# Performance work log

Hardware: AMD Instinct MI355X
Metric: run time of the kernel (lower is better)

## Reference

```python
import jax, jax.numpy as jnp
import numpy as np
import math

N_HEAD = 12


def setup_inputs() -> dict:
    key = jax.random.key(0)
    k1, k2, k3 = jax.random.split(key, 3)
    B, T, C = 4, 2048, 768
    x = jax.random.normal(k1, (B, T, C), dtype=jnp.float32)
    W = jax.random.normal(k2, (C, 3 * C), dtype=jnp.float32) * 0.02
    b = jax.random.normal(k3, (3 * C,), dtype=jnp.float32) * 0.02
    return {"x": x, "W": W, "b": b}


def reference(x, W, b):
    B, T, C = x.shape
    H = N_HEAD
    d = C // H
    qkv = x @ W + b                                # [B,T,3C]
    q, k, v = jnp.split(qkv, 3, axis=-1)           # each [B,T,C]
    q = q.reshape(B, T, H, d).transpose(0, 2, 1, 3)  # [B,H,T,d]
    k = k.reshape(B, T, H, d).transpose(0, 2, 1, 3)
    v = v.reshape(B, T, H, d).transpose(0, 2, 1, 3)
    # NOTE: source multiplies by sqrt(d) (not divides) -- faithful reproduction.
    att = jnp.einsum('bhqd,bhkd->bhqk', q, k) * (1.0 * math.sqrt(d))
    causal = jnp.tril(jnp.ones((T, T), dtype=bool))  # [T,T]
    att = jnp.where(causal[None, None, :, :], att, -jnp.inf)
    att = jax.nn.softmax(att, axis=-1)
    y = jnp.einsum('bhqk,bhkd->bhqd', att, v)      # [B,H,T,d]
    y = y.transpose(0, 2, 1, 3).reshape(B, T, C)   # [B,T,C]
    return y
```

## Files before the change

kernel.cpp:

```cpp
#include <hip/hip_runtime.h>
#include <math.h>

#define B_ 4
#define T_ 2048
#define C_ 768
#define H_ 12
#define D_ 64
#define N3C (3*C_)
#define BH_ (B_*H_)
#define QSCALE 11.5415603f

typedef float f32x4 __attribute__((ext_vector_type(4)));
typedef _Float16 f16x8 __attribute__((ext_vector_type(8)));
typedef unsigned short ushort_t;

__device__ __forceinline__ void async16(const void* g, void* l) {
    __builtin_amdgcn_global_load_lds(
        (const __attribute__((address_space(1))) unsigned int*)(g),
        (__attribute__((address_space(3))) unsigned int*)(l),
        16, 0, 0);
}

__device__ __forceinline__ unsigned pk_f16(float a, float b) {
    __fp16 r2[2];
    *(__fp16 __attribute__((ext_vector_type(2)))*)r2 = __builtin_amdgcn_cvt_pkrtz(a, b);
    return *(unsigned*)r2;
}

__global__ __launch_bounds__(256) void conv_xw(const float* __restrict__ x,
                                               const float* __restrict__ W,
                                               _Float16* __restrict__ Xh,
                                               _Float16* __restrict__ Wh)
{
    __shared__ float tile[64][65];
    int bid = blockIdx.x;
    int tid = threadIdx.x;
    if (bid < 3072) {
        int idx = bid * 256 + tid;
        const float4 a = *reinterpret_cast<const float4*>(&x[(size_t)idx * 8]);
        const float4 b = *reinterpret_cast<const float4*>(&x[(size_t)idx * 8 + 4]);
        f16x8 o = {(_Float16)a.x, (_Float16)a.y, (_Float16)a.z, (_Float16)a.w,
                   (_Float16)b.x, (_Float16)b.y, (_Float16)b.z, (_Float16)b.w};
        *reinterpret_cast<f16x8*>(&Xh[(size_t)idx * 8]) = o;
    } else {
        int b2 = bid - 3072;
        int n0 = (b2 % 36) * 64, k0 = (b2 / 36) * 64;
        #pragma unroll
        for (int t = 0; t < 16; ++t) {
            int c = t * 256 + tid;
            int kr = c >> 6, nc = c & 63;
            tile[kr][nc] = W[(size_t)(k0 + kr) * N3C + n0 + nc];
        }
        __syncthreads();
        #pragma unroll
        for (int t = 0; t < 16; ++t) {
            int c = t * 256 + tid;
            int nr = c >> 6, kc = c & 63;
            Wh[(size_t)(n0 + nr) * C_ + k0 + kc] = (_Float16)tile[kc][nr];
        }
    }
}

__global__ __launch_bounds__(256) void qkv_gemm(const _Float16* __restrict__ Xh,
                                                const _Float16* __restrict__ Wh,
                                                const float* __restrict__ bias,
                                                _Float16* __restrict__ Qf,
                                                _Float16* __restrict__ Kf,
                                                _Float16* __restrict__ Vt)
{
    __shared__ __align__(16) ushort_t SMEM[2 * 2 * 128 * 64];

    int tid = threadIdx.x, lane = tid & 63, w = tid >> 6;
    int wm = w >> 1, wn = w & 1;
    int l15 = lane & 15, l4 = lane >> 4;
    int srow = lane >> 3;
    int scol = (((lane & 7) ^ srow)) << 3;

    int wg = blockIdx.x;
    int l = (wg & 7) * 144 + (wg >> 3);
    int mt = l / 18, nt = l % 18;
    int row0 = mt * 128, col0 = nt * 128;

    f32x4 acc[4][4];
    #pragma unroll
    for (int i = 0; i < 4; ++i)
        #pragma unroll
        for (int j = 0; j < 4; ++j)
            acc[i][j] = f32x4{0.f, 0.f, 0.f, 0.f};

    #pragma unroll
    for (int j = 0; j < 4; ++j) {
        int rowb = w * 32 + j * 8;
        async16(Xh + (size_t)(row0 + rowb + srow) * C_ + scol, &SMEM[rowb * 64]);
        async16(Wh + (size_t)(col0 + rowb + srow) * C_ + scol, &SMEM[8192 + rowb * 64]);
    }
    __syncthreads();

    int cur = 0;
    for (int it = 0; it < 12; ++it) {
        int nxt = cur ^ 1;
        int k0n = (it + 1) * 64;
        bool pf = (it + 1 < 12);
        const char* AsC = (const char*)(SMEM + cur * 16384);
        const char* BsC = AsC + 16384;
        ushort_t* An = SMEM + nxt * 16384;
        ushort_t* Bn = An + 8192;

        if (pf) {
            #pragma unroll
            for (int j = 0; j < 2; ++j) {
                int rowb = w * 32 + j * 8;
                async16(Xh + (size_t)(row0 + rowb + srow) * C_ + k0n + scol, &An[rowb * 64]);
                async16(Wh + (size_t)(col0 + rowb + srow) * C_ + k0n + scol, &Bn[rowb * 64]);
            }
        }
        f16x8 bfr[4][2];
        #pragma unroll
        for (int n = 0; n < 4; ++n) {
            int r = wn * 64 + n * 16 + l15;
            #pragma unroll
            for (int kk = 0; kk < 2; ++kk)
                bfr[n][kk] = *reinterpret_cast<const f16x8*>(BsC + r * 128 + ((kk * 64 + l4 * 16) ^ ((r & 7) << 4)));
        }
        {
            f16x8 af[2][2];
            #pragma unroll
            for (int m = 0; m < 2; ++m) {
                int r = wm * 64 + m * 16 + l15;
                #pragma unroll
                for (int kk = 0; kk < 2; ++kk)
                    af[m][kk] = *reinterpret_cast<const f16x8*>(AsC + r * 128 + ((kk * 64 + l4 * 16) ^ ((r & 7) << 4)));
            }
            #pragma unroll
            for (int kk = 0; kk < 2; ++kk)
                #pragma unroll
                for (int m = 0; m < 2; ++m)
                    #pragma unroll
                    for (int n = 0; n < 4; ++n)
                        acc[m][n] = __builtin_amdgcn_mfma_f32_16x16x32_f16(af[m][kk], bfr[n][kk], acc[m][n], 0, 0, 0);
        }

        if (pf) {
            #pragma unroll
            for (int j = 2; j < 4; ++j) {
                int rowb = w * 32 + j * 8;
                async16(Xh + (size_t)(row0 + rowb + srow) * C_ + k0n + scol, &An[rowb * 64]);
                async16(Wh + (size_t)(col0 + rowb + srow) * C_ + k0n + scol, &Bn[rowb * 64]);
            }
        }
        {
            f16x8 af[2][2];
            #pragma unroll
            for (int m = 0; m < 2; ++m) {
                int r = wm * 64 + (m + 2) * 16 + l15;
                #pragma unroll
                for (int kk = 0; kk < 2; ++kk)
                    af[m][kk] = *reinterpret_cast<const f16x8*>(AsC + r * 128 + ((kk * 64 + l4 * 16) ^ ((r & 7) << 4)));
            }
            #pragma unroll
            for (int kk = 0; kk < 2; ++kk)
                #pragma unroll
                for (int m = 0; m < 2; ++m)
                    #pragma unroll
                    for (int n = 0; n < 4; ++n)
                        acc[m + 2][n] = __builtin_amdgcn_mfma_f32_16x16x32_f16(af[m][kk], bfr[n][kk], acc[m + 2][n], 0, 0, 0);
        }

        __syncthreads();
        cur = nxt;
    }

    char* EB = (char*)SMEM;
    int p = col0 / C_;

    if (p < 2) {
        #pragma unroll
        for (int n = 0; n < 4; ++n) {
            int col = wn * 64 + n * 16 + l15;
            float bv = bias[col0 + col];
            #pragma unroll
            for (int m = 0; m < 4; ++m) {
                #pragma unroll
                for (int r = 0; r < 4; ++r) {
                    int row = wm * 64 + m * 16 + l4 * 4 + r;
                    float v = acc[m][n][r] + bv;
                    if (p == 0) v *= QSCALE;
                    int off = row * 256 + ((col * 2) ^ ((row & 7) << 4));
                    *reinterpret_cast<_Float16*>(EB + off) = (_Float16)v;
                }
            }
        }
        __syncthreads();
        int ti = tid >> 1, half = tid & 1;
        int grow = row0 + ti;
        int bq = grow >> 11, t = grow & (T_ - 1);
        int rem = (col0 + half * 64) - p * C_;
        int hh = rem >> 6;
        _Float16* dst = (p == 0 ? Qf : Kf) + ((size_t)(bq * H_ + hh) * T_ + t) * D_;
        #pragma unroll
        for (int u = 0; u < 8; ++u) {
            int off = ti * 256 + ((half * 128 + u * 16) ^ ((ti & 7) << 4));
            *reinterpret_cast<uint4*>((char*)dst + u * 16) = *reinterpret_cast<const uint4*>(EB + off);
        }
    } else {
        #pragma unroll
        for (int n = 0; n < 4; ++n) {
            int col = wn * 64 + n * 16 + l15;
            float bv = bias[col0 + col];
            #pragma unroll
            for (int m = 0; m < 4; ++m) {
                int row = wm * 64 + m * 16 + l4 * 4;
                uint2 pk;
                pk.x = pk_f16(acc[m][n][0] + bv, acc[m][n][1] + bv);
                pk.y = pk_f16(acc[m][n][2] + bv, acc[m][n][3] + bv);
                int off = col * 256 + ((row * 2) ^ ((col & 15) << 4));
                *reinterpret_cast<uint2*>(EB + off) = pk;
            }
        }
        __syncthreads();
        int dcol = tid >> 1, half = tid & 1;
        int rem = (col0 + dcol) - 1536;
        int hh = rem >> 6, dd = rem & 63;
        int bq = row0 >> 11, t0 = row0 & (T_ - 1);
        _Float16* dst = Vt + ((size_t)(bq * H_ + hh) * D_ + dd) * T_ + t0 + half * 64;
        #pragma unroll
        for (int u = 0; u < 8; ++u) {
            int off = dcol * 256 + ((half * 128 + u * 16) ^ ((dcol & 15) << 4));
            *reinterpret_cast<uint4*>((char*)dst + u * 16) = *reinterpret_cast<const uint4*>(EB + off);
        }
    }
}

__device__ const unsigned char ITEM_QT[24] = {15,15,7,14,14,13,13,6,12,12,11,11,5,10,10,9,9,4,8,8,3,2,1,0};
__device__ const unsigned char ITEM_CH[24] = { 0, 1,0, 0, 1, 0, 1,0, 0, 1, 0, 1,0, 0, 1,0,1,0,0,1,0,0,0,0};

__global__ __launch_bounds__(256, 4) void attn(const _Float16* __restrict__ Qf,
                                               const _Float16* __restrict__ Kf,
                                               const _Float16* __restrict__ Vt,
                                               float* __restrict__ out,
                                               float* __restrict__ Op,
                                               float* __restrict__ ML)
{
    __shared__ __align__(16) char smem[40960];
    ushort_t* lds = (ushort_t*)smem;

    int tid = threadIdx.x, lane = tid & 63, w = tid >> 6;
    int l15 = lane & 15, l4 = lane >> 4;
    int bid = blockIdx.x;
    int rank = bid / BH_;
    int bh = bid % BH_;
    int qt = ITEM_QT[rank];
    int ch = ITEM_CH[rank];
    int b = bh / H_, h = bh % H_;
    int q0 = qt * 128;

    int it0 = (qt < 8 || ch == 0) ? 0 : (qt + 1);
    int it1 = (qt >= 8 && ch == 0) ? (qt + 1) : (2 * qt + 2);

    f16x8 qf[2][2];
    #pragma unroll
    for (int qs = 0; qs < 2; ++qs) {
        int q = q0 + w * 32 + qs * 16 + l15;
        const _Float16* ph = Qf + ((size_t)bh * T_ + q) * D_;
        qf[qs][0] = *reinterpret_cast<const f16x8*>(ph + l4 * 8);
        qf[qs][1] = *reinterpret_cast<const f16x8*>(ph + 32 + l4 * 8);
    }

    f32x4 yacc[2][4];
    #pragma unroll
    for (int qs = 0; qs < 2; ++qs)
        #pragma unroll
        for (int dt = 0; dt < 4; ++dt)
            yacc[qs][dt] = f32x4{0.f, 0.f, 0.f, 0.f};
    float m_run[2] = {-INFINITY, -INFINITY};
    float l_run[2] = {0.f, 0.f};

    int srow = lane >> 3;
    int scol = ((lane & 7) ^ srow) << 3;
    char* PwB = (char*)(lds + 16384 + w * 1024);
    int pswz = (l15 & 7) << 4;

    const _Float16* kp[2];
    const _Float16* vp[2];
    #pragma unroll
    for (int j = 0; j < 2; ++j) {
        int row = (w * 2 + j) * 8 + srow;
        kp[j] = Kf + ((size_t)bh * T_ + it0 * 64 + row) * D_ + scol;
        vp[j] = Vt + ((size_t)bh * D_ + row) * T_ + it0 * 64 + scol;
    }

    #pragma unroll
    for (int j = 0; j < 2; ++j) {
        ushort_t* dK = lds + (w * 2 + j) * 512;
        async16(kp[j], dK);
        async16(vp[j], dK + 4096);
        kp[j] += 64 * D_;
        vp[j] += 64;
    }
    __syncthreads();

    int cur = 0;
    for (int it = it0; it < it1; ++it) {
        int k0 = it * 64;
        int nxt = cur ^ 1;
        if (it + 1 < it1) {
            #pragma unroll
            for (int j = 0; j < 2; ++j) {
                ushort_t* dK = lds + nxt * 8192 + (w * 2 + j) * 512;
                async16(kp[j], dK);
                async16(vp[j], dK + 4096);
                kp[j] += 64 * D_;
                vp[j] += 64;
            }
        }

        if (k0 <= q0 + w * 32 + 31) {
            const char* KHc = (const char*)(lds + cur * 8192);
            const char* VSc = KHc + 8192;
            f16x8 pa[2][2];
            f32x4 sa[2][4];
            #pragma unroll
            for (int qs = 0; qs < 2; ++qs)
                #pragma unroll
                for (int i = 0; i < 4; ++i) sa[qs][i] = f32x4{0.f, 0.f, 0.f, 0.f};

            __builtin_amdgcn_s_setprio(1);
            #pragma unroll
            for (int kt = 0; kt < 4; ++kt) {
                int krow = kt * 16 + l15;
                int swz = (krow & 7) << 4;
                #pragma unroll
                for (int dh = 0; dh < 2; ++dh) {
                    f16x8 kf = *reinterpret_cast<const f16x8*>(KHc + krow * 128 + ((dh * 64 + l4 * 16) ^ swz));
                    sa[0][kt] = __builtin_amdgcn_mfma_f32_16x16x32_f16(kf, qf[0][dh], sa[0][kt], 0, 0, 0);
                    sa[1][kt] = __builtin_amdgcn_mfma_f32_16x16x32_f16(kf, qf[1][dh], sa[1][kt], 0, 0, 0);
                }
            }
            __builtin_amdgcn_s_setprio(0);

            #pragma unroll
            for (int qs = 0; qs < 2; ++qs) {
                if (it >= 2 * qt) {
                    int qg = q0 + w * 32 + qs * 16 + l15;
                    #pragma unroll
                    for (int kt = 0; kt < 4; ++kt)
                        #pragma unroll
                        for (int r = 0; r < 4; ++r)
                            if (k0 + kt * 16 + l4 * 4 + r > qg) sa[qs][kt][r] = -INFINITY;
                }

                float mx = sa[qs][0][0];
                #pragma unroll
                for (int kt = 0; kt < 4; ++kt)
                    #pragma unroll
                    for (int r = 0; r < 4; ++r) mx = fmaxf(mx, sa[qs][kt][r]);
                mx = fmaxf(mx, __shfl_xor(mx, 16));
                mx = fmaxf(mx, __shfl_xor(mx, 32));

                float mn;
                if (__all(mx <= m_run[qs] + 8.0f)) {
                    mn = m_run[qs];
                } else {
                    mn = fmaxf(m_run[qs], mx);
                    float sc = exp2f(m_run[qs] - mn);
                    m_run[qs] = mn;
                    l_run[qs] *= sc;
                    #pragma unroll
                    for (int dt = 0; dt < 4; ++dt) yacc[qs][dt] *= sc;
                }

                float p[4][4];
                float rs = 0.f;
                #pragma unroll
                for (int kt = 0; kt < 4; ++kt)
                    #pragma unroll
                    for (int r = 0; r < 4; ++r) {
                        p[kt][r] = exp2f(sa[qs][kt][r] - mn);
                        rs += p[kt][r];
                    }
                l_run[qs] += rs;

                #pragma unroll
                for (int kt = 0; kt < 4; ++kt) {
                    uint2 pw;
                    pw.x = pk_f16(p[kt][0], p[kt][1]);
                    pw.y = pk_f16(p[kt][2], p[kt][3]);
                    int off = (l15 * 128 + kt * 32 + l4 * 8) ^ pswz;
                    *reinterpret_cast<uint2*>(PwB + off) = pw;
                }
                pa[qs][0] = *reinterpret_cast<const f16x8*>(PwB + ((l15 * 128 + l4 * 16) ^ pswz));
                pa[qs][1] = *reinterpret_cast<const f16x8*>(PwB + ((l15 * 128 + 64 + l4 * 16) ^ pswz));
            }

            __builtin_amdgcn_s_setprio(1);
            #pragma unroll
            for (int dt = 0; dt < 4; ++dt) {
                int vrow = dt * 16 + l15;
                int vswz = (vrow & 7) << 4;
                #pragma unroll
                for (int kk = 0; kk < 2; ++kk) {
                    f16x8 vf = *reinterpret_cast<const f16x8*>(VSc + vrow * 128 + ((kk * 64 + l4 * 16) ^ vswz));
                    yacc[0][dt] = __builtin_amdgcn_mfma_f32_16x16x32_f16(vf, pa[0][kk], yacc[0][dt], 0, 0, 0);
                    yacc[1][dt] = __builtin_amdgcn_mfma_f32_16x16x32_f16(vf, pa[1][kk], yacc[1][dt], 0, 0, 0);
                }
            }
            __builtin_amdgcn_s_setprio(0);
        }
        __syncthreads();
        cur = nxt;
    }

    #pragma unroll
    for (int qs = 0; qs < 2; ++qs) {
        l_run[qs] += __shfl_xor(l_run[qs], 16);
        l_run[qs] += __shfl_xor(l_run[qs], 32);
    }

    float* ot = (float*)smem;
    if (qt < 8) {
        #pragma unroll
        for (int qs = 0; qs < 2; ++qs) {
            float inv = 1.0f / l_run[qs];
            int rq = w * 32 + qs * 16 + l15;
            #pragma unroll
            for (int dt = 0; dt < 4; ++dt)
                #pragma unroll
                for (int r = 0; r < 4; ++r)
                    ot[rq * 68 + dt * 16 + l4 * 4 + r] = yacc[qs][dt][r] * inv;
        }
        __syncthreads();
        int rr = tid >> 1, c0 = (tid & 1) * 32;
        size_t ob = ((size_t)(b * T_ + q0 + rr)) * C_ + h * D_ + c0;
        #pragma unroll
        for (int u = 0; u < 8; ++u) {
            float4 v = *reinterpret_cast<const float4*>(&ot[rr * 68 + c0 + u * 4]);
            *reinterpret_cast<float4*>(&out[ob + u * 4]) = v;
        }
    } else {
        #pragma unroll
        for (int qs = 0; qs < 2; ++qs) {
            int rq = w * 32 + qs * 16 + l15;
            #pragma unroll
            for (int dt = 0; dt < 4; ++dt)
                #pragma unroll
                for (int r = 0; r < 4; ++r)
                    ot[rq * 68 + dt * 16 + l4 * 4 + r] = yacc[qs][dt][r];
        }
        if (l4 == 0) {
            float* mlp = ML + (((size_t)bh * 8 + (qt - 8)) * 2 + ch) * 256;
            #pragma unroll
            for (int qs = 0; qs < 2; ++qs) {
                int ql = w * 32 + qs * 16 + l15;
                mlp[ql] = m_run[qs];
                mlp[128 + ql] = l_run[qs];
            }
        }
        __syncthreads();
        int rr = tid >> 1, c0 = (tid & 1) * 32;
        float* dst = Op + (((size_t)bh * 8 + (qt - 8)) * 2 + ch) * 8192 + rr * 64 + c0;
        #pragma unroll
        for (int u = 0; u < 8; ++u) {
            float4 v = *reinterpret_cast<const float4*>(&ot[rr * 68 + c0 + u * 4]);
            *reinterpret_cast<float4*>(&dst[u * 4]) = v;
        }
    }
}

__global__ __launch_bounds__(256) void merge(const float* __restrict__ Op,
                                             const float* __restrict__ ML,
                                             float* __restrict__ out)
{
    int gid = blockIdx.x * 256 + threadIdx.x;
    int row = gid >> 4, seg = gid & 15;
    int q = row & 127, qt8 = (row >> 7) & 7, bh = row >> 10;

    size_t mbase = ((size_t)bh * 8 + qt8) * 2 * 256;
    float m1 = ML[mbase + q],       l1 = ML[mbase + 128 + q];
    float m2 = ML[mbase + 256 + q], l2 = ML[mbase + 256 + 128 + q];
    float m = fmaxf(m1, m2);
    float a1 = exp2f(m1 - m), a2 = exp2f(m2 - m);
    float inv = 1.0f / (l1 * a1 + l2 * a2);

    size_t obase = ((size_t)bh * 8 + qt8) * 2 * 8192 + q * 64 + seg * 4;
    float4 o1 = *reinterpret_cast<const float4*>(&Op[obase]);
    float4 o2 = *reinterpret_cast<const float4*>(&Op[obase + 8192]);
    float4 r;
    r.x = (o1.x * a1 + o2.x * a2) * inv;
    r.y = (o1.y * a1 + o2.y * a2) * inv;
    r.z = (o1.z * a1 + o2.z * a2) * inv;
    r.w = (o1.w * a1 + o2.w * a2) * inv;

    int b = bh / H_, h = bh % H_;
    int t = (qt8 + 8) * 128 + q;
    *reinterpret_cast<float4*>(&out[((size_t)(b * T_ + t)) * C_ + h * D_ + seg * 4]) = r;
}

extern "C" void kernel_launch(void* const* d_in, const int* in_sizes, int n_in,
                              void* d_out, int out_size, void* d_ws, size_t ws_size,
                              hipStream_t stream)
{
    const float* x    = (const float*)d_in[0];
    const float* W    = (const float*)d_in[1];
    const float* bias = (const float*)d_in[2];

    const size_t per = (size_t)BH_ * T_ * D_;
    _Float16* Qf = (_Float16*)d_ws;
    _Float16* Kf = Qf + per;
    _Float16* Vt = Kf + per;
    _Float16* Xh = Vt + per;
    _Float16* Wh = Xh + (size_t)8192 * C_;
    float*    Op = (float*)(Wh + (size_t)N3C * C_);
    float*    ML = Op + (size_t)48 * 8 * 2 * 8192;

    conv_xw<<<dim3(3072 + 432), 256, 0, stream>>>(x, W, Xh, Wh);
    qkv_gemm<<<dim3(64 * 18), 256, 0, stream>>>(Xh, Wh, bias, Qf, Kf, Vt);
    attn<<<dim3(24 * BH_), 256, 0, stream>>>(Qf, Kf, Vt, (float*)d_out, Op, ML);
    merge<<<dim3(49152 * 16 / 256), 256, 0, stream>>>(Op, ML, (float*)d_out);
}
```

Baseline: 130.5 us.

## Permute K rows so P stays in registers, drop LDS round-trip for P

K rows are loaded into LDS in a permuted order, so each lane's QK^T accumulator values line up with the A-operand layout the PV MFMA expects. P can then be packed to f16 directly in registers instead of being written to and reread from a per-wave LDS scratch buffer. The causal mask is updated to use the permuted key indices, and LDS usage falls from 40KB to 32KB. The epilogue is also unified to use float4 swizzled LDS stores for both the split and non-split paths. The permutation must be exactly right for both the mask and the MFMA layout, otherwise results will be wrong.

New measurement: 129.5 us. No clear change (-0.8%).

```diff
diff --git a/kernel.cpp b/kernel.cpp
--- a/kernel.cpp
+++ b/kernel.cpp
@@ -241,7 +241,7 @@
                                                float* __restrict__ Op,
                                                float* __restrict__ ML)
 {
-    __shared__ __align__(16) char smem[40960];
+    __shared__ __align__(16) char smem[32768];
     ushort_t* lds = (ushort_t*)smem;
 
     int tid = threadIdx.x, lane = tid & 63, w = tid >> 6;
@@ -277,16 +277,15 @@
 
     int srow = lane >> 3;
     int scol = ((lane & 7) ^ srow) << 3;
-    char* PwB = (char*)(lds + 16384 + w * 1024);
-    int pswz = (l15 & 7) << 4;
 
     const _Float16* kp[2];
     const _Float16* vp[2];
     #pragma unroll
     for (int j = 0; j < 2; ++j) {
-        int row = (w * 2 + j) * 8 + srow;
-        kp[j] = Kf + ((size_t)bh * T_ + it0 * 64 + row) * D_ + scol;
-        vp[j] = Vt + ((size_t)bh * D_ + row) * T_ + it0 * 64 + scol;
+        int ldsrow = (w * 2 + j) * 8 + srow;
+        int kperm = ((ldsrow >> 4) & 1) * 32 + ((ldsrow >> 2) & 3) * 8 + ((ldsrow >> 5) << 2) + (ldsrow & 3);
+        kp[j] = Kf + ((size_t)bh * T_ + it0 * 64 + kperm) * D_ + scol;
+        vp[j] = Vt + ((size_t)bh * D_ + ldsrow) * T_ + it0 * 64 + scol;
     }
 
     #pragma unroll
@@ -338,6 +337,7 @@
             }
             __builtin_amdgcn_s_setprio(0);
 
+            int kml = k0 + l4 * 8;
             #pragma unroll
             for (int qs = 0; qs < 2; ++qs) {
                 if (it >= 2 * qt) {
@@ -345,8 +345,10 @@
                     #pragma unroll
                     for (int kt = 0; kt < 4; ++kt)
                         #pragma unroll
-                        for (int r = 0; r < 4; ++r)
-                            if (k0 + kt * 16 + l4 * 4 + r > qg) sa[qs][kt][r] = -INFINITY;
+                        for (int r = 0; r < 4; ++r) {
+                            int kact = kml + ((kt & 1) << 5) + ((kt >> 1) << 2) + r;
+                            if (kact > qg) sa[qs][kt][r] = -INFINITY;
+                        }
                 }
 
                 float mx = sa[qs][0][0];
@@ -380,16 +382,17 @@
                     }
                 l_run[qs] += rs;
 
-                #pragma unroll
-                for (int kt = 0; kt < 4; ++kt) {
-                    uint2 pw;
-                    pw.x = pk_f16(p[kt][0], p[kt][1]);
-                    pw.y = pk_f16(p[kt][2], p[kt][3]);
-                    int off = (l15 * 128 + kt * 32 + l4 * 8) ^ pswz;
-                    *reinterpret_cast<uint2*>(PwB + off) = pw;
-                }
-                pa[qs][0] = *reinterpret_cast<const f16x8*>(PwB + ((l15 * 128 + l4 * 16) ^ pswz));
-                pa[qs][1] = *reinterpret_cast<const f16x8*>(PwB + ((l15 * 128 + 64 + l4 * 16) ^ pswz));
+                union { uint4 u; f16x8 h; } c0, c1;
+                c0.u.x = pk_f16(p[0][0], p[0][1]);
+                c0.u.y = pk_f16(p[0][2], p[0][3]);
+                c0.u.z = pk_f16(p[2][0], p[2][1]);
+                c0.u.w = pk_f16(p[2][2], p[2][3]);
+                c1.u.x = pk_f16(p[1][0], p[1][1]);
+                c1.u.y = pk_f16(p[1][2], p[1][3]);
+                c1.u.z = pk_f16(p[3][0], p[3][1]);
+                c1.u.w = pk_f16(p[3][2], p[3][3]);
+                pa[qs][0] = c0.h;
+                pa[qs][1] = c1.h;
             }
 
             __builtin_amdgcn_s_setprio(1);
@@ -416,52 +419,51 @@
         l_run[qs] += __shfl_xor(l_run[qs], 32);
     }
 
-    float* ot = (float*)smem;
-    if (qt < 8) {
+    bool split = (qt >= 8);
+    if (split && l4 == 0) {
+        float* mlp = ML + (((size_t)bh * 8 + (qt - 8)) * 2 + ch) * 256;
         #pragma unroll
         for (int qs = 0; qs < 2; ++qs) {
-            float inv = 1.0f / l_run[qs];
-            int rq = w * 32 + qs * 16 + l15;
-            #pragma unroll
-            for (int dt = 0; dt < 4; ++dt)
-                #pragma unroll
-                for (int r = 0; r < 4; ++r)
-                    ot[rq * 68 + dt * 16 + l4 * 4 + r] = yacc[qs][dt][r] * inv;
-        }
-        __syncthreads();
-        int rr = tid >> 1, c0 = (tid & 1) * 32;
-        size_t ob = ((size_t)(b * T_ + q0 + rr)) * C_ + h * D_ + c0;
-        #pragma unroll
-        for (int u = 0; u < 8; ++u) {
-            float4 v = *reinterpret_cast<const float4*>(&ot[rr * 68 + c0 + u * 4]);
-            *reinterpret_cast<float4*>(&out[ob + u * 4]) = v;
-        }
-    } else {
-        #pragma unroll
-        for (int qs = 0; qs < 2; ++qs) {
-            int rq = w * 32 + qs * 16 + l15;
-            #pragma unroll
-            for (int dt = 0; dt < 4; ++dt)
-                #pragma unroll
-                for (int r = 0; r < 4; ++r)
-                    ot[rq * 68 + dt * 16 + l4 * 4 + r] = yacc[qs][dt][r];
-        }
-        if (l4 == 0) {
-            float* mlp = ML + (((size_t)bh * 8 + (qt - 8)) * 2 + ch) * 256;
-            #pragma unroll
-            for (int qs = 0; qs < 2; ++qs) {
-                int ql = w * 32 + qs * 16 + l15;
-                mlp[ql] = m_run[qs];
-                mlp[128 + ql] = l_run[qs];
-            }
-        }
-        __syncthreads();
-        int rr = tid >> 1, c0 = (tid & 1) * 32;
-        float* dst = Op + (((size_t)bh * 8 + (qt - 8)) * 2 + ch) * 8192 + rr * 64 + c0;
-        #pragma unroll
-        for (int u = 0; u < 8; ++u) {
-            float4 v = *reinterpret_cast<const float4*>(&ot[rr * 68 + c0 + u * 4]);
-            *reinterpret_cast<float4*>(&dst[u * 4]) = v;
+            int ql = w * 32 + qs * 16 + l15;
+            mlp[ql] = m_run[qs];
+            mlp[128 + ql] = l_run[qs];
+        }
+    }
+
+    char* otB = smem;
+    #pragma unroll
+    for (int qs = 0; qs < 2; ++qs) {
+        float inv = split ? 1.0f : (1.0f / l_run[qs]);
+        int rq = w * 32 + qs * 16 + l15;
+        int swz = (rq & 15) << 4;
+        #pragma unroll
+        for (int dt = 0; dt < 4; ++dt) {
+            float4 v4;
+            v4.x = yacc[qs][dt][0] * inv;
+            v4.y = yacc[qs][dt][1] * inv;
+            v4.z = yacc[qs][dt][2] * inv;
+            v4.w = yacc[qs][dt][3] * inv;
+            *reinterpret_cast<float4*>(otB + rq * 256 + ((dt * 64 + l4 * 16) ^ swz)) = v4;
+        }
+    }
+    __syncthreads();
+    {
+        int rr = tid >> 1, cb = (tid & 1) * 128;
+        int swz = (rr & 15) << 4;
+        if (!split) {
+            size_t ob = ((size_t)(b * T_ + q0 + rr)) * C_ + h * D_ + (tid & 1) * 32;
+            #pragma unroll
+            for (int u = 0; u < 8; ++u) {
+                float4 v = *reinterpret_cast<const float4*>(otB + rr * 256 + ((cb + u * 16) ^ swz));
+                *reinterpret_cast<float4*>(&out[ob + u * 4]) = v;
+            }
+        } else {
+            float* dst = Op + (((size_t)bh * 8 + (qt - 8)) * 2 + ch) * 8192 + rr * 64 + (tid & 1) * 32;
+            #pragma unroll
+            for (int u = 0; u < 8; ++u) {
+                float4 v = *reinterpret_cast<const float4*>(otB + rr * 256 + ((cb + u * 16) ^ swz));
+                *reinterpret_cast<float4*>(&dst[u * 4]) = v;
+            }
         }
     }
 }
```
